# Optimization experiments

Measured on AMD Instinct MI355X. Metric: run time of the kernel, lower is better.

The kernel has to match this reference:

```python
import jax, jax.numpy as jnp
import numpy as np

B, L, DP, DS = 8, 256, 128, 256  # batch, length, d_pair, d_seq (= 2*d_pair)
NEAR = 4
K = 3  # k_base=3 (no trbv emb); full mask + 2 chains => every row valid


def _ln(x, g, b):
    mu = x.mean(-1, keepdims=True)
    var = ((x - mu) ** 2).mean(-1, keepdims=True)
    return (x - mu) / jnp.sqrt(var + 1e-5) * g + b


def _masked_mean(x, m, axes):
    num = (x * m).sum(axes)
    den = jnp.clip(m.sum(axes), 1e-6, None)
    return num / den


def _masked_max(x, m, axes):
    v = jnp.where(m > 0, x, -jnp.inf).max(axes)
    return jnp.where(jnp.isinf(v), jnp.zeros_like(v), v)


def _mlp(x, w1, b1, w2, b2):
    return jax.nn.relu(x @ w1 + b1) @ w2 + b2


def setup_inputs() -> dict:
    key = jax.random.key(0)
    ks = jax.random.split(key, 26)
    s = 0.02
    d = {
        "seq_repr": jax.random.normal(ks[0], (B, L, DS), jnp.float32),
        "pair_repr": jax.random.normal(ks[1], (B, L, L, DP), jnp.float32),
        "chain_id": jax.random.randint(ks[2], (B, L), 0, 2, jnp.int32),
        "mask": jnp.ones((B, L), jnp.bool_),
        "ln_s_g": jnp.ones((DS,), jnp.float32),
        "ln_s_b": jnp.zeros((DS,), jnp.float32),
        "ln_z_g": jnp.ones((DS,), jnp.float32),
        "ln_z_b": jnp.zeros((DS,), jnp.float32),
        "W_seq": jax.random.normal(ks[3], (DS, DS), jnp.float32) * s,
        "W_pair": jax.random.normal(ks[4], (DS, DS), jnp.float32) * s,
    }
    in_dim = 2 * DS
    for i, name in enumerate(["m0", "m1", "m2"]):
        d[name + "_w1"] = jax.random.normal(ks[5 + 4 * i], (in_dim, 64), jnp.float32) * s
        d[name + "_b1"] = jnp.zeros((64,), jnp.float32)
        d[name + "_w2"] = jax.random.normal(ks[6 + 4 * i], (64, 1), jnp.float32) * s
        d[name + "_b2"] = jnp.zeros((1,), jnp.float32)
    d["f_w1"] = jax.random.normal(ks[20], (3, 8), jnp.float32) * s
    d["f_b1"] = jnp.zeros((8,), jnp.float32)
    d["f_w2"] = jax.random.normal(ks[21], (8, 1), jnp.float32) * s
    d["f_b2"] = jnp.zeros((1,), jnp.float32)
    return d


def reference(seq_repr, pair_repr, chain_id, mask,
              ln_s_g, ln_s_b, ln_z_g, ln_z_b, W_seq, W_pair,
              m0_w1, m0_b1, m0_w2, m0_b2,
              m1_w1, m1_b1, m1_w2, m1_b2,
              m2_w1, m2_b1, m2_w2, m2_b2,
              f_w1, f_b1, f_w2, f_b2):
    m = mask.astype(jnp.float32)[..., None]  # [B,L,1]
    s = _ln(seq_repr, ln_s_g, ln_s_b) @ W_seq  # [B,L,DS]
    s_mean = _masked_mean(s, m, 1)
    s_max = _masked_max(s, m, 1)
    s_feat = jnp.concatenate([s_mean, s_max], -1)  # [B,2*DS]

    pair = jnp.concatenate([pair_repr, jnp.swapaxes(pair_repr, 1, 2)], -1)  # [B,L,L,DS]
    eye = jnp.eye(L, dtype=pair.dtype)[None, :, :, None]
    pair = pair * (1.0 - eye)
    z = _ln(pair, ln_z_g, ln_z_b) @ W_pair  # [B,L,L,DS]

    pm = (mask[:, :, None] & mask[:, None, :]).astype(jnp.float32)[..., None]  # [B,L,L,1]
    same = (chain_id[:, :, None] == chain_id[:, None, :])[..., None]
    intra = pm * same.astype(jnp.float32)
    inter = pm * (~same).astype(jnp.float32)

    inter_mean = _masked_mean(z, inter, (1, 2))  # [B,DS]
    row_den_raw = inter.sum(2)  # [B,L,1]
    row_valid = row_den_raw[..., 0] > 0
    row_mean_i = (z * inter).sum(2) / jnp.clip(row_den_raw, 1e-6, None)  # [B,L,DS]
    score = jnp.where(row_valid, jnp.linalg.norm(row_mean_i, axis=-1), -1e9)
    _, topk_idx = jax.lax.top_k(score, K)  # [B,K]
    selected = jnp.take_along_axis(row_mean_i, topk_idx[..., None], axis=1)
    inter_peak = selected.mean(1)
    inter_feat = jnp.concatenate([inter_mean, inter_peak], -1)

    idx = jnp.arange(L)
    diff = jnp.abs(idx[:, None] - idx[None, :])
    band = ((diff <= NEAR) & (diff > 0)).astype(jnp.float32)[None, :, :, None]
    intra_near = intra * band
    intra_compact = _masked_mean(z, intra_near, (1, 2))
    intra_max = _masked_max(z, intra_near, (1, 2))
    intra_feat = jnp.concatenate([intra_compact, intra_max], -1)

    logits = jnp.concatenate([
        _mlp(s_feat, m0_w1, m0_b1, m0_w2, m0_b2),
        _mlp(inter_feat, m1_w1, m1_b1, m1_w2, m1_b2),
        _mlp(intra_feat, m2_w1, m2_b1, m2_w2, m2_b2),
    ], axis=1)  # [B,3]
    return jax.nn.relu(logits @ f_w1 + f_b1) @ f_w2 + f_b2  # [B,1]
```

## Files before the change

### kernel.cpp

```cpp
#include <hip/hip_runtime.h>
#include <math.h>

#define NB 8
#define NL 256
#define NDP 128
#define NDS 256
#define NEARB 4


__device__ __forceinline__ float waveSum(float v) {
#pragma unroll
  for (int m = 1; m < 64; m <<= 1) v += __shfl_xor(v, m);
  return v;
}

__device__ __forceinline__ void waveSum2(float& a, float& b) {
#pragma unroll
  for (int m = 1; m < 64; m <<= 1) {
    a += __shfl_xor(a, m);
    b += __shfl_xor(b, m);
  }
}

__device__ __forceinline__ void grpSum2(float& a, float& b) {
#pragma unroll
  for (int m = 1; m < 32; m <<= 1) {
    a += __shfl_xor(a, m);
    b += __shfl_xor(b, m);
  }
}

__device__ __forceinline__ void grpSum4(float& a, float& b, float& c,
                                        float& d) {
#pragma unroll
  for (int m = 1; m < 32; m <<= 1) {
    a += __shfl_xor(a, m);
    b += __shfl_xor(b, m);
    c += __shfl_xor(c, m);
    d += __shfl_xor(d, m);
  }
}

__global__ __launch_bounds__(256) void kA_pair(
    const float* __restrict__ pair, const int* __restrict__ chain,
    const float* __restrict__ g, const float* __restrict__ beta,
    const float* __restrict__ Wp, float* __restrict__ acc,
    float* __restrict__ cntI, float* __restrict__ intraLN,
    float* __restrict__ cntA, float* __restrict__ bandMax) {
  const int i = blockIdx.x;
  const int b = blockIdx.y;
  const int tid = threadIdx.x;
  const int wave = tid >> 6, lane = tid & 63;
  const int grp = lane >> 5, pos = lane & 31;
  const int slot = wave * 2 + grp;

  __shared__ int sList[NL];
  __shared__ int sCnt4[4];
  __shared__ int sOff[4];
  __shared__ int sN;
  __shared__ float sAcc[8][NDS];
  __shared__ float lnrow[8][NDS];

  const int ci = chain[b * NL + i];

  {
    const bool flag = (chain[b * NL + tid] != ci);
    unsigned long long bal = __ballot(flag);
    int ppos = __popcll(bal & ((1ull << lane) - 1ull));
    if (lane == 0) sCnt4[wave] = __popcll(bal);
    __syncthreads();
    if (tid == 0) {
      int o = 0;
#pragma unroll
      for (int w = 0; w < 4; ++w) {
        sOff[w] = o;
        o += sCnt4[w];
      }
      sN = o;
    }
    __syncthreads();
    if (flag) sList[sOff[wave] + ppos] = tid;
    __syncthreads();

    const int n = sN;
    const int c0 = 8 * pos;
    const float4 gA = *(const float4*)(g + c0);
    const float4 gB = *(const float4*)(g + c0 + 4);
    const float4 bA = *(const float4*)(beta + c0);
    const float4 bB = *(const float4*)(beta + c0 + 4);

    const bool rowHalf = (pos < 16);
    const float* sb = rowHalf ? pair + ((size_t)(b * NL + i) * NL) * NDP + c0
                              : pair + ((size_t)b * NL * NL) * NDP +
                                    (size_t)i * NDP + (c0 - NDP);
    const size_t jstr = rowHalf ? (size_t)NDP : (size_t)NL * NDP;

    float r0 = 0.f, r1 = 0.f, r2 = 0.f, r3 = 0.f;
    float r4 = 0.f, r5 = 0.f, r6 = 0.f, r7 = 0.f;

    int p = slot;
    for (; p + 8 < n; p += 16) {
      const int jX = sList[p];
      const int jY = sList[p + 8];
      const float* srcX = sb + (size_t)jX * jstr;
      const float* srcY = sb + (size_t)jY * jstr;
      float4 x0 = *(const float4*)srcX;
      float4 x1 = *(const float4*)(srcX + 4);
      float4 y0 = *(const float4*)srcY;
      float4 y1 = *(const float4*)(srcY + 4);
      float sX = (x0.x + x0.y) + (x0.z + x0.w) + (x1.x + x1.y) + (x1.z + x1.w);
      float ssX = x0.x * x0.x + x0.y * x0.y + x0.z * x0.z + x0.w * x0.w +
                  x1.x * x1.x + x1.y * x1.y + x1.z * x1.z + x1.w * x1.w;
      float sY = (y0.x + y0.y) + (y0.z + y0.w) + (y1.x + y1.y) + (y1.z + y1.w);
      float ssY = y0.x * y0.x + y0.y * y0.y + y0.z * y0.z + y0.w * y0.w +
                  y1.x * y1.x + y1.y * y1.y + y1.z * y1.z + y1.w * y1.w;
      grpSum4(sX, ssX, sY, ssY);
      const float muX = sX * (1.0f / NDS);
      const float invX = 1.0f / sqrtf(ssX * (1.0f / NDS) - muX * muX + 1e-5f);
      const float muY = sY * (1.0f / NDS);
      const float invY = 1.0f / sqrtf(ssY * (1.0f / NDS) - muY * muY + 1e-5f);
      r0 += (x0.x - muX) * invX * gA.x + bA.x;
      r1 += (x0.y - muX) * invX * gA.y + bA.y;
      r2 += (x0.z - muX) * invX * gA.z + bA.z;
      r3 += (x0.w - muX) * invX * gA.w + bA.w;
      r4 += (x1.x - muX) * invX * gB.x + bB.x;
      r5 += (x1.y - muX) * invX * gB.y + bB.y;
      r6 += (x1.z - muX) * invX * gB.z + bB.z;
      r7 += (x1.w - muX) * invX * gB.w + bB.w;
      r0 += (y0.x - muY) * invY * gA.x + bA.x;
      r1 += (y0.y - muY) * invY * gA.y + bA.y;
      r2 += (y0.z - muY) * invY * gA.z + bA.z;
      r3 += (y0.w - muY) * invY * gA.w + bA.w;
      r4 += (y1.x - muY) * invY * gB.x + bB.x;
      r5 += (y1.y - muY) * invY * gB.y + bB.y;
      r6 += (y1.z - muY) * invY * gB.z + bB.z;
      r7 += (y1.w - muY) * invY * gB.w + bB.w;
    }
    for (; p < n; p += 8) {
      const int j = sList[p];
      const float* src = sb + (size_t)j * jstr;
      float4 a0 = *(const float4*)src;
      float4 a1 = *(const float4*)(src + 4);
      float s = (a0.x + a0.y) + (a0.z + a0.w) + (a1.x + a1.y) + (a1.z + a1.w);
      float ss = a0.x * a0.x + a0.y * a0.y + a0.z * a0.z + a0.w * a0.w +
                 a1.x * a1.x + a1.y * a1.y + a1.z * a1.z + a1.w * a1.w;
      grpSum2(s, ss);
      float mu = s * (1.0f / NDS);
      float inv = 1.0f / sqrtf(ss * (1.0f / NDS) - mu * mu + 1e-5f);
      r0 += (a0.x - mu) * inv * gA.x + bA.x;
      r1 += (a0.y - mu) * inv * gA.y + bA.y;
      r2 += (a0.z - mu) * inv * gA.z + bA.z;
      r3 += (a0.w - mu) * inv * gA.w + bA.w;
      r4 += (a1.x - mu) * inv * gB.x + bB.x;
      r5 += (a1.y - mu) * inv * gB.y + bB.y;
      r6 += (a1.z - mu) * inv * gB.z + bB.z;
      r7 += (a1.w - mu) * inv * gB.w + bB.w;
    }

    *(float4*)&sAcc[slot][c0] = make_float4(r0, r1, r2, r3);
    *(float4*)&sAcc[slot][c0 + 4] = make_float4(r4, r5, r6, r7);
    __syncthreads();
    float v = 0.f;
#pragma unroll
    for (int p2 = 0; p2 < 8; ++p2) v += sAcc[p2][tid];
    acc[(size_t)(b * NL + i) * NDS + tid] = v;
    if (tid == 0) cntI[b * NL + i] = (float)n;
  }

  {
    const int t = tid;
    int js[8];
    int nv = 0;
    for (int dj = -NEARB; dj <= NEARB; ++dj) {
      int j = i + dj;
      if (dj == 0 || j < 0 || j >= NL) continue;
      if (chain[b * NL + j] == ci) js[nv++] = j;
    }

    const int c0 = 4 * lane;
    const float4 g4 = *(const float4*)(g + c0);
    const float4 b4 = *(const float4*)(beta + c0);
    for (int r = wave; r < 8; r += 4) {
      if (r < nv) {
        const int j = js[r];
        const float* src =
            (lane < 32)
                ? pair + ((size_t)(b * NL + i) * NL + j) * NDP + c0
                : pair + ((size_t)(b * NL + j) * NL + i) * NDP + (c0 - NDP);
        float4 a = *(const float4*)src;
        float s = (a.x + a.y) + (a.z + a.w);
        float ss = a.x * a.x + a.y * a.y + a.z * a.z + a.w * a.w;
        waveSum2(s, ss);
        float mu = s * (1.0f / NDS);
        float inv = 1.0f / sqrtf(ss * (1.0f / NDS) - mu * mu + 1e-5f);
        lnrow[r][c0] = (a.x - mu) * inv * g4.x + b4.x;
        lnrow[r][c0 + 1] = (a.y - mu) * inv * g4.y + b4.y;
        lnrow[r][c0 + 2] = (a.z - mu) * inv * g4.z + b4.z;
        lnrow[r][c0 + 3] = (a.w - mu) * inv * g4.w + b4.w;
      } else {
        lnrow[r][c0] = 0.f;
        lnrow[r][c0 + 1] = 0.f;
        lnrow[r][c0 + 2] = 0.f;
        lnrow[r][c0 + 3] = 0.f;
      }
    }
    __syncthreads();

    float z[8] = {0, 0, 0, 0, 0, 0, 0, 0};
    if (nv > 0) {
      for (int k = 0; k < NDS; ++k) {
        float wk = Wp[k * NDS + t];
#pragma unroll
        for (int r = 0; r < 8; ++r) z[r] += lnrow[r][k] * wk;
      }
    }
    float zmax = -INFINITY, lnsum = 0.f;
#pragma unroll
    for (int r = 0; r < 8; ++r)
      if (r < nv) {
        zmax = fmaxf(zmax, z[r]);
        lnsum += lnrow[r][t];
      }
    intraLN[(size_t)(b * NL + i) * NDS + t] = lnsum;
    bandMax[(size_t)(b * NL + i) * NDS + t] = zmax;
    if (t == 0) cntA[b * NL + i] = (float)nv;
  }
}

__global__ __launch_bounds__(256) void k3_seq(const float* __restrict__ seq,
                                              const float* __restrict__ g,
                                              const float* __restrict__ beta,
                                              const float* __restrict__ Ws,
                                              float* __restrict__ sbuf) {
  const int chunk = blockIdx.x;
  const int b = blockIdx.y;
  const int t = threadIdx.x;
  const int wave = t >> 6, lane = t & 63;
  __shared__ float lnrow[4][NDS];

  const int c0 = 4 * lane;
  const float4 g4 = *(const float4*)(g + c0);
  const float4 b4 = *(const float4*)(beta + c0);
  {
    const int r = wave;
    const int l = chunk * 4 + r;
    float4 a = *(const float4*)(seq + (size_t)(b * NL + l) * NDS + c0);
    float s = (a.x + a.y) + (a.z + a.w);
    float ss = a.x * a.x + a.y * a.y + a.z * a.z + a.w * a.w;
    waveSum2(s, ss);
    float mu = s * (1.0f / NDS);
    float inv = 1.0f / sqrtf(ss * (1.0f / NDS) - mu * mu + 1e-5f);
    lnrow[r][c0] = (a.x - mu) * inv * g4.x + b4.x;
    lnrow[r][c0 + 1] = (a.y - mu) * inv * g4.y + b4.y;
    lnrow[r][c0 + 2] = (a.z - mu) * inv * g4.z + b4.z;
    lnrow[r][c0 + 3] = (a.w - mu) * inv * g4.w + b4.w;
  }
  __syncthreads();
  float z[4] = {0, 0, 0, 0};
  for (int k = 0; k < NDS; ++k) {
    float wk = Ws[k * NDS + t];
#pragma unroll
    for (int r = 0; r < 4; ++r) z[r] += lnrow[r][k] * wk;
  }
#pragma unroll
  for (int r = 0; r < 4; ++r)
    sbuf[(size_t)(b * NL + chunk * 4 + r) * NDS + t] = z[r];
}

__global__ __launch_bounds__(256) void kB_rowmean(
    const float* __restrict__ acc, const float* __restrict__ cntI,
    const float* __restrict__ Wp, const float* __restrict__ sbuf,
    const float* __restrict__ intraLN, const float* __restrict__ cntA,
    const float* __restrict__ bandMax, float* __restrict__ rmean,
    float* __restrict__ score, float* __restrict__ part,
    float* __restrict__ partC) {
  const int chunk = blockIdx.x;
  const int b = blockIdx.y;
  const int t = threadIdx.x;
  const int wave = t >> 6, lane = t & 63;
  __shared__ float vrow[4][NDS];
  __shared__ float red[4];
  float cnts[4], araw[4];
#pragma unroll
  for (int r = 0; r < 4; ++r) {
    const int i = chunk * 4 + r;
    float c = cntI[b * NL + i];
    cnts[r] = c;
    araw[r] = acc[(size_t)(b * NL + i) * NDS + t];
    vrow[r][t] = araw[r] / fmaxf(c, 1e-6f);
  }
  __syncthreads();
  float z[4] = {0, 0, 0, 0};
  for (int k = 0; k < NDS; ++k) {
    float wk = Wp[k * NDS + t];
#pragma unroll
    for (int r = 0; r < 4; ++r) z[r] += vrow[r][k] * wk;
  }
#pragma unroll
  for (int r = 0; r < 4; ++r) {
    const int i = chunk * 4 + r;
    rmean[(size_t)(b * NL + i) * NDS + t] = z[r];
    float q = waveSum(z[r] * z[r]);
    __syncthreads();
    if (lane == 0) red[wave] = q;
    __syncthreads();
    if (t == 0) {
      float ss = red[0] + red[1] + red[2] + red[3];
      score[b * NL + i] = (cnts[r] > 0.f) ? sqrtf(ss) : -1e9f;
    }
    __syncthreads();
  }

  float ssum = 0.f, smax = -INFINITY, isum = 0.f, imax = -INFINITY;
  const float asum = araw[0] + araw[1] + araw[2] + araw[3];
#pragma unroll
  for (int r = 0; r < 4; ++r) {
    const size_t idx = (size_t)(b * NL + chunk * 4 + r) * NDS + t;
    float v = sbuf[idx];
    ssum += v;
    smax = fmaxf(smax, v);
    isum += intraLN[idx];
    imax = fmaxf(imax, bandMax[idx]);
  }
  const size_t pb = (size_t)(b * 64 + chunk) * 5 * NDS;
  part[pb + 0 * NDS + t] = ssum;
  part[pb + 1 * NDS + t] = smax;
  part[pb + 2 * NDS + t] = asum;
  part[pb + 3 * NDS + t] = isum;
  part[pb + 4 * NDS + t] = imax;
  if (t == 0) {
    partC[(b * 64 + chunk) * 2 + 0] = cnts[0] + cnts[1] + cnts[2] + cnts[3];
    float ia = 0.f;
    for (int r = 0; r < 4; ++r) ia += cntA[b * NL + chunk * 4 + r];
    partC[(b * 64 + chunk) * 2 + 1] = ia;
  }
}

__global__ __launch_bounds__(256) void kC_heads(
    const float* __restrict__ part, const float* __restrict__ partC,
    const float* __restrict__ Wp, const float* __restrict__ score,
    const float* __restrict__ rmean, const float* __restrict__ m0w1,
    const float* __restrict__ m0b1, const float* __restrict__ m0w2,
    const float* __restrict__ m0b2, const float* __restrict__ m1w1,
    const float* __restrict__ m1b1, const float* __restrict__ m1w2,
    const float* __restrict__ m1b2, const float* __restrict__ m2w1,
    const float* __restrict__ m2b1, const float* __restrict__ m2w2,
    const float* __restrict__ m2b2, float* __restrict__ logitsBuf) {
  const int b = blockIdx.x;
  const int q = blockIdx.y;
  const int t = threadIdx.x;
  __shared__ float f[2 * NDS];
  __shared__ float sv[NDS];
  __shared__ float hp[4][64];
  __shared__ float h[64];
  __shared__ float sc[NL];
  __shared__ float rv[NL];
  __shared__ int ri[NL];
  __shared__ int top3[3];

  if (q == 0) {
    float ssum = 0.f, smax = -INFINITY;
    for (int c = 0; c < 64; ++c) {
      const size_t pb = (size_t)(b * 64 + c) * 5 * NDS;
      ssum += part[pb + 0 * NDS + t];
      smax = fmaxf(smax, part[pb + 1 * NDS + t]);
    }
    f[t] = ssum * (1.0f / NL);
    f[NDS + t] = isinf(smax) ? 0.f : smax;
    __syncthreads();
  } else if (q == 1) {
    float asum = 0.f, tc = 0.f;
    for (int c = 0; c < 64; ++c) {
      asum += part[(size_t)(b * 64 + c) * 5 * NDS + 2 * NDS + t];
      tc += partC[(b * 64 + c) * 2 + 0];
    }
    sv[t] = asum / fmaxf(tc, 1e-6f);
    sc[t] = score[b * NL + t];
    __syncthreads();
    float om = 0.f;
    for (int k = 0; k < NDS; ++k) om += sv[k] * Wp[k * NDS + t];
    f[t] = om;
    for (int r = 0; r < 3; ++r) {
      rv[t] = sc[t];
      ri[t] = t;
      __syncthreads();
      for (int s2 = 128; s2 > 0; s2 >>= 1) {
        if (t < s2) {
          if (rv[t + s2] > rv[t] ||
              (rv[t + s2] == rv[t] && ri[t + s2] < ri[t])) {
            rv[t] = rv[t + s2];
            ri[t] = ri[t + s2];
          }
        }
        __syncthreads();
      }
      if (t == 0) {
        top3[r] = ri[0];
        sc[ri[0]] = -INFINITY;
      }
      __syncthreads();
    }
    const int i0 = top3[0], i1 = top3[1], i2 = top3[2];
    f[NDS + t] = (rmean[(size_t)(b * NL + i0) * NDS + t] +
                  rmean[(size_t)(b * NL + i1) * NDS + t] +
                  rmean[(size_t)(b * NL + i2) * NDS + t]) *
                 (1.0f / 3.0f);
    __syncthreads();
  } else {
    float isum = 0.f, ic = 0.f, imax = -INFINITY;
    for (int c = 0; c < 64; ++c) {
      const size_t pb = (size_t)(b * 64 + c) * 5 * NDS;
      isum += part[pb + 3 * NDS + t];
      imax = fmaxf(imax, part[pb + 4 * NDS + t]);
      ic += partC[(b * 64 + c) * 2 + 1];
    }
    sv[t] = isum / fmaxf(ic, 1e-6f);
    __syncthreads();
    float oc = 0.f;
    for (int k = 0; k < NDS; ++k) oc += sv[k] * Wp[k * NDS + t];
    f[t] = oc;
    f[NDS + t] = isinf(imax) ? 0.f : imax;
    __syncthreads();
  }

  const float* w1 = (q == 0) ? m0w1 : ((q == 1) ? m1w1 : m2w1);
  const float* b1 = (q == 0) ? m0b1 : ((q == 1) ? m1b1 : m2b1);
  const float* w2 = (q == 0) ? m0w2 : ((q == 1) ? m1w2 : m2w2);
  const float* b2 = (q == 0) ? m0b2 : ((q == 1) ? m1b2 : m2b2);
  const int o = t & 63, c4 = t >> 6;
  float a = 0.f;
  for (int k = c4 * 128; k < c4 * 128 + 128; ++k) a += f[k] * w1[k * 64 + o];
  hp[c4][o] = a;
  __syncthreads();
  if (t < 64)
    h[t] = fmaxf(hp[0][t] + hp[1][t] + hp[2][t] + hp[3][t] + b1[t], 0.f);
  __syncthreads();
  if (t < 64) {
    float p = h[t] * w2[t];
    p = waveSum(p);
    if (t == 0) logitsBuf[b * 3 + q] = p + b2[0];
  }
}

__global__ __launch_bounds__(64) void kD_final(
    const float* __restrict__ logitsBuf, const float* __restrict__ fw1,
    const float* __restrict__ fb1, const float* __restrict__ fw2,
    const float* __restrict__ fb2, float* __restrict__ out) {
  const int t = threadIdx.x;
  if (t < NB) {
    float l0 = logitsBuf[t * 3 + 0];
    float l1 = logitsBuf[t * 3 + 1];
    float l2 = logitsBuf[t * 3 + 2];
    float o = 0.f;
    for (int u = 0; u < 8; ++u) {
      float a = fb1[u] + l0 * fw1[0 * 8 + u] + l1 * fw1[1 * 8 + u] +
                l2 * fw1[2 * 8 + u];
      o += fmaxf(a, 0.f) * fw2[u];
    }
    out[t] = o + fb2[0];
  }
}

extern "C" void kernel_launch(void* const* d_in, const int* in_sizes, int n_in,
                              void* d_out, int out_size, void* d_ws,
                              size_t ws_size, hipStream_t stream) {
  const float* seq = (const float*)d_in[0];
  const float* pair = (const float*)d_in[1];
  const int* chain = (const int*)d_in[2];
  const float* ln_s_g = (const float*)d_in[4];
  const float* ln_s_b = (const float*)d_in[5];
  const float* ln_z_g = (const float*)d_in[6];
  const float* ln_z_b = (const float*)d_in[7];
  const float* Ws = (const float*)d_in[8];
  const float* Wp = (const float*)d_in[9];
  const float* m0w1 = (const float*)d_in[10];
  const float* m0b1 = (const float*)d_in[11];
  const float* m0w2 = (const float*)d_in[12];
  const float* m0b2 = (const float*)d_in[13];
  const float* m1w1 = (const float*)d_in[14];
  const float* m1b1 = (const float*)d_in[15];
  const float* m1w2 = (const float*)d_in[16];
  const float* m1b2 = (const float*)d_in[17];
  const float* m2w1 = (const float*)d_in[18];
  const float* m2b1 = (const float*)d_in[19];
  const float* m2w2 = (const float*)d_in[20];
  const float* m2b2 = (const float*)d_in[21];
  const float* fw1 = (const float*)d_in[22];
  const float* fb1 = (const float*)d_in[23];
  const float* fw2 = (const float*)d_in[24];
  const float* fb2 = (const float*)d_in[25];
  float* out = (float*)d_out;

  float* ws = (float*)d_ws;
  float* acc = ws;
  float* cntI = acc + (size_t)NB * NL * NDS;
  float* sbuf = cntI + NB * NL;
  float* intraLN = sbuf + (size_t)NB * NL * NDS;
  float* cntA = intraLN + (size_t)NB * NL * NDS;
  float* bandMax = cntA + NB * NL;
  float* rmean = bandMax + (size_t)NB * NL * NDS;
  float* score = rmean + (size_t)NB * NL * NDS;
  float* part = score + NB * NL;
  float* partC = part + (size_t)NB * 64 * 5 * NDS;
  float* logitsBuf = partC + NB * 64 * 2;

  kA_pair<<<dim3(NL, NB), 256, 0, stream>>>(pair, chain, ln_z_g, ln_z_b, Wp,
                                            acc, cntI, intraLN, cntA,
                                            bandMax);
  k3_seq<<<dim3(NL / 4, NB), 256, 0, stream>>>(seq, ln_s_g, ln_s_b, Ws, sbuf);
  kB_rowmean<<<dim3(NL / 4, NB), 256, 0, stream>>>(acc, cntI, Wp, sbuf,
                                                   intraLN, cntA, bandMax,
                                                   rmean, score, part, partC);
  kC_heads<<<dim3(NB, 3), 256, 0, stream>>>(part, partC, Wp, score, rmean,
                                            m0w1, m0b1, m0w2, m0b2, m1w1,
                                            m1b1, m1w2, m1b2, m2w1, m2b1,
                                            m2w2, m2b2, logitsBuf);
  kD_final<<<1, 64, 0, stream>>>(logitsBuf, fw1, fb1, fw2, fb2, out);
}
```

Baseline: 128.8 us.

## Factor LayerNorm affine out of pair sum and fuse seq projection into rowmean

The inter-chain pair accumulation now sums x*inv and mu*inv per row and applies gamma and beta once at the end, which removes the per-element affine work in the hot loop. The 2x unrolled loop is dropped in favour of a single loop. The separate seq LayerNorm/projection kernel is merged into kB_rowmean, so one launch and the sbuf write/read round-trip disappear. In exchange the merged kernel does two matvecs per k step and uses more shared memory, and losing the unroll may reduce memory-level parallelism in kA.

Result: slower. 135.5 us (+5.1%).

```diff
diff --git a/kernel.cpp b/kernel.cpp
--- a/kernel.cpp
+++ b/kernel.cpp
@@ -27,17 +27,6 @@
   for (int m = 1; m < 32; m <<= 1) {
     a += __shfl_xor(a, m);
     b += __shfl_xor(b, m);
-  }
-}
-
-__device__ __forceinline__ void grpSum4(float& a, float& b, float& c,
-                                        float& d) {
-#pragma unroll
-  for (int m = 1; m < 32; m <<= 1) {
-    a += __shfl_xor(a, m);
-    b += __shfl_xor(b, m);
-    c += __shfl_xor(c, m);
-    d += __shfl_xor(d, m);
   }
 }
 
@@ -59,6 +48,7 @@
   __shared__ int sOff[4];
   __shared__ int sN;
   __shared__ float sAcc[8][NDS];
+  __shared__ float sU[8];
   __shared__ float lnrow[8][NDS];
 
   const int ci = chain[b * NL + i];
@@ -84,10 +74,6 @@
 
     const int n = sN;
     const int c0 = 8 * pos;
-    const float4 gA = *(const float4*)(g + c0);
-    const float4 gB = *(const float4*)(g + c0 + 4);
-    const float4 bA = *(const float4*)(beta + c0);
-    const float4 bB = *(const float4*)(beta + c0 + 4);
 
     const bool rowHalf = (pos < 16);
     const float* sb = rowHalf ? pair + ((size_t)(b * NL + i) * NL) * NDP + c0
@@ -95,48 +81,11 @@
                                     (size_t)i * NDP + (c0 - NDP);
     const size_t jstr = rowHalf ? (size_t)NDP : (size_t)NL * NDP;
 
-    float r0 = 0.f, r1 = 0.f, r2 = 0.f, r3 = 0.f;
-    float r4 = 0.f, r5 = 0.f, r6 = 0.f, r7 = 0.f;
-
-    int p = slot;
-    for (; p + 8 < n; p += 16) {
-      const int jX = sList[p];
-      const int jY = sList[p + 8];
-      const float* srcX = sb + (size_t)jX * jstr;
-      const float* srcY = sb + (size_t)jY * jstr;
-      float4 x0 = *(const float4*)srcX;
-      float4 x1 = *(const float4*)(srcX + 4);
-      float4 y0 = *(const float4*)srcY;
-      float4 y1 = *(const float4*)(srcY + 4);
-      float sX = (x0.x + x0.y) + (x0.z + x0.w) + (x1.x + x1.y) + (x1.z + x1.w);
-      float ssX = x0.x * x0.x + x0.y * x0.y + x0.z * x0.z + x0.w * x0.w +
-                  x1.x * x1.x + x1.y * x1.y + x1.z * x1.z + x1.w * x1.w;
-      float sY = (y0.x + y0.y) + (y0.z + y0.w) + (y1.x + y1.y) + (y1.z + y1.w);
-      float ssY = y0.x * y0.x + y0.y * y0.y + y0.z * y0.z + y0.w * y0.w +
-                  y1.x * y1.x + y1.y * y1.y + y1.z * y1.z + y1.w * y1.w;
-      grpSum4(sX, ssX, sY, ssY);
-      const float muX = sX * (1.0f / NDS);
-      const float invX = 1.0f / sqrtf(ssX * (1.0f / NDS) - muX * muX + 1e-5f);
-      const float muY = sY * (1.0f / NDS);
-      const float invY = 1.0f / sqrtf(ssY * (1.0f / NDS) - muY * muY + 1e-5f);
-      r0 += (x0.x - muX) * invX * gA.x + bA.x;
-      r1 += (x0.y - muX) * invX * gA.y + bA.y;
-      r2 += (x0.z - muX) * invX * gA.z + bA.z;
-      r3 += (x0.w - muX) * invX * gA.w + bA.w;
-      r4 += (x1.x - muX) * invX * gB.x + bB.x;
-      r5 += (x1.y - muX) * invX * gB.y + bB.y;
-      r6 += (x1.z - muX) * invX * gB.z + bB.z;
-      r7 += (x1.w - muX) * invX * gB.w + bB.w;
-      r0 += (y0.x - muY) * invY * gA.x + bA.x;
-      r1 += (y0.y - muY) * invY * gA.y + bA.y;
-      r2 += (y0.z - muY) * invY * gA.z + bA.z;
-      r3 += (y0.w - muY) * invY * gA.w + bA.w;
-      r4 += (y1.x - muY) * invY * gB.x + bB.x;
-      r5 += (y1.y - muY) * invY * gB.y + bB.y;
-      r6 += (y1.z - muY) * invY * gB.z + bB.z;
-      r7 += (y1.w - muY) * invY * gB.w + bB.w;
-    }
-    for (; p < n; p += 8) {
+    float R0 = 0.f, R1 = 0.f, R2 = 0.f, R3 = 0.f;
+    float R4 = 0.f, R5 = 0.f, R6 = 0.f, R7 = 0.f;
+    float U = 0.f;
+
+    for (int p = slot; p < n; p += 8) {
       const int j = sList[p];
       const float* src = sb + (size_t)j * jstr;
       float4 a0 = *(const float4*)src;
@@ -145,25 +94,29 @@
       float ss = a0.x * a0.x + a0.y * a0.y + a0.z * a0.z + a0.w * a0.w +
                  a1.x * a1.x + a1.y * a1.y + a1.z * a1.z + a1.w * a1.w;
       grpSum2(s, ss);
-      float mu = s * (1.0f / NDS);
-      float inv = 1.0f / sqrtf(ss * (1.0f / NDS) - mu * mu + 1e-5f);
-      r0 += (a0.x - mu) * inv * gA.x + bA.x;
-      r1 += (a0.y - mu) * inv * gA.y + bA.y;
-      r2 += (a0.z - mu) * inv * gA.z + bA.z;
-      r3 += (a0.w - mu) * inv * gA.w + bA.w;
-      r4 += (a1.x - mu) * inv * gB.x + bB.x;
-      r5 += (a1.y - mu) * inv * gB.y + bB.y;
-      r6 += (a1.z - mu) * inv * gB.z + bB.z;
-      r7 += (a1.w - mu) * inv * gB.w + bB.w;
-    }
-
-    *(float4*)&sAcc[slot][c0] = make_float4(r0, r1, r2, r3);
-    *(float4*)&sAcc[slot][c0 + 4] = make_float4(r4, r5, r6, r7);
+      const float mu = s * (1.0f / NDS);
+      const float inv = 1.0f / sqrtf(ss * (1.0f / NDS) - mu * mu + 1e-5f);
+      R0 = fmaf(a0.x, inv, R0);
+      R1 = fmaf(a0.y, inv, R1);
+      R2 = fmaf(a0.z, inv, R2);
+      R3 = fmaf(a0.w, inv, R3);
+      R4 = fmaf(a1.x, inv, R4);
+      R5 = fmaf(a1.y, inv, R5);
+      R6 = fmaf(a1.z, inv, R6);
+      R7 = fmaf(a1.w, inv, R7);
+      U = fmaf(mu, inv, U);
+    }
+
+    *(float4*)&sAcc[slot][c0] = make_float4(R0, R1, R2, R3);
+    *(float4*)&sAcc[slot][c0 + 4] = make_float4(R4, R5, R6, R7);
+    sU[slot] = U;
     __syncthreads();
     float v = 0.f;
 #pragma unroll
     for (int p2 = 0; p2 < 8; ++p2) v += sAcc[p2][tid];
-    acc[(size_t)(b * NL + i) * NDS + tid] = v;
+    float Utot = sU[0] + sU[1] + sU[2] + sU[3] + sU[4] + sU[5] + sU[6] + sU[7];
+    acc[(size_t)(b * NL + i) * NDS + tid] =
+        g[tid] * (v - Utot) + (float)n * beta[tid];
     if (tid == 0) cntI[b * NL + i] = (float)n;
   }
 
@@ -227,21 +180,34 @@
   }
 }
 
-__global__ __launch_bounds__(256) void k3_seq(const float* __restrict__ seq,
-                                              const float* __restrict__ g,
-                                              const float* __restrict__ beta,
-                                              const float* __restrict__ Ws,
-                                              float* __restrict__ sbuf) {
+__global__ __launch_bounds__(256) void kB_rowmean(
+    const float* __restrict__ acc, const float* __restrict__ cntI,
+    const float* __restrict__ Wp, const float* __restrict__ seq,
+    const float* __restrict__ gs, const float* __restrict__ bs,
+    const float* __restrict__ Ws, const float* __restrict__ intraLN,
+    const float* __restrict__ cntA, const float* __restrict__ bandMax,
+    float* __restrict__ rmean, float* __restrict__ score,
+    float* __restrict__ part, float* __restrict__ partC) {
   const int chunk = blockIdx.x;
   const int b = blockIdx.y;
   const int t = threadIdx.x;
   const int wave = t >> 6, lane = t & 63;
-  __shared__ float lnrow[4][NDS];
-
-  const int c0 = 4 * lane;
-  const float4 g4 = *(const float4*)(g + c0);
-  const float4 b4 = *(const float4*)(beta + c0);
+  __shared__ float vrow[4][NDS];
+  __shared__ float srow[4][NDS];
+  __shared__ float red[4];
+  float cnts[4], araw[4];
+#pragma unroll
+  for (int r = 0; r < 4; ++r) {
+    const int i = chunk * 4 + r;
+    float c = cntI[b * NL + i];
+    cnts[r] = c;
+    araw[r] = acc[(size_t)(b * NL + i) * NDS + t];
+    vrow[r][t] = araw[r] / fmaxf(c, 1e-6f);
+  }
   {
+    const int c0 = 4 * lane;
+    const float4 g4 = *(const float4*)(gs + c0);
+    const float4 b4 = *(const float4*)(bs + c0);
     const int r = wave;
     const int l = chunk * 4 + r;
     float4 a = *(const float4*)(seq + (size_t)(b * NL + l) * NDS + c0);
@@ -250,51 +216,22 @@
     waveSum2(s, ss);
     float mu = s * (1.0f / NDS);
     float inv = 1.0f / sqrtf(ss * (1.0f / NDS) - mu * mu + 1e-5f);
-    lnrow[r][c0] = (a.x - mu) * inv * g4.x + b4.x;
-    lnrow[r][c0 + 1] = (a.y - mu) * inv * g4.y + b4.y;
-    lnrow[r][c0 + 2] = (a.z - mu) * inv * g4.z + b4.z;
-    lnrow[r][c0 + 3] = (a.w - mu) * inv * g4.w + b4.w;
+    srow[r][c0] = (a.x - mu) * inv * g4.x + b4.x;
+    srow[r][c0 + 1] = (a.y - mu) * inv * g4.y + b4.y;
+    srow[r][c0 + 2] = (a.z - mu) * inv * g4.z + b4.z;
+    srow[r][c0 + 3] = (a.w - mu) * inv * g4.w + b4.w;
   }
   __syncthreads();
   float z[4] = {0, 0, 0, 0};
+  float z2[4] = {0, 0, 0, 0};
   for (int k = 0; k < NDS; ++k) {
-    float wk = Ws[k * NDS + t];
-#pragma unroll
-    for (int r = 0; r < 4; ++r) z[r] += lnrow[r][k] * wk;
-  }
-#pragma unroll
-  for (int r = 0; r < 4; ++r)
-    sbuf[(size_t)(b * NL + chunk * 4 + r) * NDS + t] = z[r];
-}
-
-__global__ __launch_bounds__(256) void kB_rowmean(
-    const float* __restrict__ acc, const float* __restrict__ cntI,
-    const float* __restrict__ Wp, const float* __restrict__ sbuf,
-    const float* __restrict__ intraLN, const float* __restrict__ cntA,
-    const float* __restrict__ bandMax, float* __restrict__ rmean,
-    float* __restrict__ score, float* __restrict__ part,
-    float* __restrict__ partC) {
-  const int chunk = blockIdx.x;
-  const int b = blockIdx.y;
-  const int t = threadIdx.x;
-  const int wave = t >> 6, lane = t & 63;
-  __shared__ float vrow[4][NDS];
-  __shared__ float red[4];
-  float cnts[4], araw[4];
-#pragma unroll
-  for (int r = 0; r < 4; ++r) {
-    const int i = chunk * 4 + r;
-    float c = cntI[b * NL + i];
-    cnts[r] = c;
-    araw[r] = acc[(size_t)(b * NL + i) * NDS + t];
-    vrow[r][t] = araw[r] / fmaxf(c, 1e-6f);
-  }
-  __syncthreads();
-  float z[4] = {0, 0, 0, 0};
-  for (int k = 0; k < NDS; ++k) {
-    float wk = Wp[k * NDS + t];
-#pragma unroll
-    for (int r = 0; r < 4; ++r) z[r] += vrow[r][k] * wk;
+    float wkp = Wp[k * NDS + t];
+    float wks = Ws[k * NDS + t];
+#pragma unroll
+    for (int r = 0; r < 4; ++r) {
+      z[r] += vrow[r][k] * wkp;
+      z2[r] += srow[r][k] * wks;
+    }
   }
 #pragma unroll
   for (int r = 0; r < 4; ++r) {
@@ -311,14 +248,13 @@
     __syncthreads();
   }
 
-  float ssum = 0.f, smax = -INFINITY, isum = 0.f, imax = -INFINITY;
+  const float ssum = z2[0] + z2[1] + z2[2] + z2[3];
+  const float smax = fmaxf(fmaxf(z2[0], z2[1]), fmaxf(z2[2], z2[3]));
   const float asum = araw[0] + araw[1] + araw[2] + araw[3];
+  float isum = 0.f, imax = -INFINITY;
 #pragma unroll
   for (int r = 0; r < 4; ++r) {
     const size_t idx = (size_t)(b * NL + chunk * 4 + r) * NDS + t;
-    float v = sbuf[idx];
-    ssum += v;
-    smax = fmaxf(smax, v);
     isum += intraLN[idx];
     imax = fmaxf(imax, bandMax[idx]);
   }
@@ -494,8 +430,7 @@
   float* ws = (float*)d_ws;
   float* acc = ws;
   float* cntI = acc + (size_t)NB * NL * NDS;
-  float* sbuf = cntI + NB * NL;
-  float* intraLN = sbuf + (size_t)NB * NL * NDS;
+  float* intraLN = cntI + NB * NL;
   float* cntA = intraLN + (size_t)NB * NL * NDS;
   float* bandMax = cntA + NB * NL;
   float* rmean = bandMax + (size_t)NB * NL * NDS;
@@ -507,10 +442,9 @@
   kA_pair<<<dim3(NL, NB), 256, 0, stream>>>(pair, chain, ln_z_g, ln_z_b, Wp,
                                             acc, cntI, intraLN, cntA,
                                             bandMax);
-  k3_seq<<<dim3(NL / 4, NB), 256, 0, stream>>>(seq, ln_s_g, ln_s_b, Ws, sbuf);
-  kB_rowmean<<<dim3(NL / 4, NB), 256, 0, stream>>>(acc, cntI, Wp, sbuf,
-                                                   intraLN, cntA, bandMax,
-                                                   rmean, score, part, partC);
+  kB_rowmean<<<dim3(NL / 4, NB), 256, 0, stream>>>(
+      acc, cntI, Wp, seq, ln_s_g, ln_s_b, Ws, intraLN, cntA, bandMax, rmean,
+      score, part, partC);
   kC_heads<<<dim3(NB, 3), 256, 0, stream>>>(part, partC, Wp, score, rmean,
                                             m0w1, m0b1, m0w2, m0b2, m1w1,
                                             m1b1, m1w2, m1b2, m2w1, m2b1,
```
